# Kernel tuning notes

Hardware: AMD Instinct MI355X
Metric: run time of the kernel (lower is better)

The kernel has to match this reference:

```python
import jax, jax.numpy as jnp
import numpy as np

# pywt db4 reconstruction low-pass (rec_lo) coefficients.
_H = np.array([
    0.23037781330885523, 0.7148465705525415, 0.6308807679295904,
    -0.02798376941698385, -0.18703481171888114, 0.030841381835986965,
    0.032883011666982945, -0.010597401784997278], dtype=np.float64)
# pywt dec_lo = _H[::-1]; conv (flipped) correlation kernel = dec_lo[::-1] = _H.
_FLO = _H
# dec_hi[k] = (-1)^(7-k) * _H[k]; correlation kernel = dec_hi[::-1] -> (-1)^k * _H[7-k].
_FHI = np.array([(-1.0) ** k * _H[7 - k] for k in range(8)])
_FILT = jnp.asarray(np.stack([_FLO, _FHI])[:, None, :], dtype=jnp.float32)  # [2,1,8]
_PAD = 7  # filter_len - 1
_LEVEL = 4


def _dwt_step(sig):
    """One pywt dwt level, mode='symmetric'. sig: [N, L] -> (cA, cD), each [N, (L+7)//2]."""
    # symmetric (half-sample) extension by filter_len-1 each side, drop first sample
    # so that stride-2 VALID correlation reproduces pywt's output phase/length.
    xp = jnp.pad(sig, ((0, 0), (_PAD, _PAD)), mode='symmetric')[:, 1:]
    out = jax.lax.conv_general_dilated(
        xp[:, None, :], _FILT, window_strides=(2,), padding='VALID',
        dimension_numbers=('NCH', 'OIH', 'NCH'))  # [N, 2, (L+7)//2]
    return out[:, 0, :], out[:, 1, :]


def setup_inputs() -> dict:
    key = jax.random.key(0)
    x = jax.random.normal(key, (64, 4096, 32), dtype=jnp.float32)  # [B, L, C]
    return {"x": x}


def reference(x):
    """Faithful batched version of pywt.wavedec(x[i,:,j], 'db4', 'symmetric', level=4).
    Returns tuple (cA4, cD4, cD3, cD2, cD1), each [B, C, scale_len]."""
    B, L, C = x.shape
    sig = jnp.transpose(x, (0, 2, 1)).reshape(B * C, L)
    details = []
    for _ in range(_LEVEL):
        sig, cd = _dwt_step(sig)
        details.append(cd)
    coeffs = [sig] + details[::-1]  # [cA_L, cD_L, ..., cD_1] like pywt.wavedec
    return tuple(c.reshape(B, C, c.shape[-1]) for c in coeffs)
```

## Files before the change

### kernel.cpp

```cpp
#include <hip/hip_runtime.h>


#define NCH 8

__device__ __forceinline__ int sym_idx(int t, int L) {
    if (t < 0) t = -1 - t;
    if (t >= L) t = 2 * L - 1 - t;
    return t;
}

__device__ __forceinline__ void level_step(
    const float* __restrict__ src, int src_base, int srcL,
    float* __restrict__ dst, int dst_base,
    int lo, int hi,
    float* __restrict__ cdRow, int ownLo, int ownHi,
    float* __restrict__ caRow,
    int c, int slot) {
    constexpr float FLO[8] = {
        0.23037781330885523f,  0.7148465705525415f,  0.6308807679295904f,
        -0.02798376941698385f, -0.18703481171888114f, 0.030841381835986965f,
        0.032883011666982945f, -0.010597401784997278f};
    constexpr float FHI[8] = {
        -0.010597401784997278f, -0.032883011666982945f, 0.030841381835986965f,
        0.18703481171888114f,  -0.02798376941698385f,  -0.6308807679295904f,
        0.7148465705525415f,   -0.23037781330885523f};

    for (int i = lo + slot; i < hi; i += 32) {
        float a = 0.f, d = 0.f;
#pragma unroll
        for (int k = 0; k < 8; ++k) {
            int t = sym_idx(2 * i - 6 + k, srcL);
            const float v = src[(t - src_base) * NCH + c];
            a = fmaf(FLO[k], v, a);
            d = fmaf(FHI[k], v, d);
        }
        if (dst) dst[(i - dst_base) * NCH + c] = a;
        if (caRow) caRow[i] = a;
        if (i >= ownLo && i < ownHi) cdRow[i] = d;
    }
}

__global__ __launch_bounds__(256) void fused_dwt_kernel(
    const float* __restrict__ x, float* __restrict__ out) {
    const int bid = blockIdx.x;
    const int work = (bid & 7) * 256 + (bid >> 3);
    const int cg = work & 3;
    const int tile = (work >> 2) & 7;
    const int b = work >> 5;

    const int tid = threadIdx.x;
    const int c = tid & 7;
    const int slot = tid >> 3;
    const int c0 = cg * 8;

    const int L0 = 4096, L1 = 2051, L2 = 1029, L3 = 518, L4 = 262;

    const int lo4 = tile * 33, hi4 = min(L4, lo4 + 33);
    const int lo3 = max(0, 2 * lo4 - 6), hi3 = min(L3, 2 * hi4);
    const int lo2 = max(0, 2 * lo3 - 6), hi2 = min(L2, 2 * hi3);
    const int lo1 = max(0, 2 * lo2 - 6), hi1 = min(L1, 2 * hi2);
    const int lox = max(0, 2 * lo1 - 6), hix = min(L0, 2 * hi1);

    __shared__ float bx[618 * NCH];
    __shared__ float b1[306 * NCH];
    __shared__ float b2[150 * NCH];
    __shared__ float b3[72 * NCH];

    const float* xb = x + (size_t)b * L0 * 32 + c0;
    const int nx = hix - lox;
    for (int q = tid; q < nx * 2; q += 256) {
        const int jj = q >> 1;
        const int h = (q & 1) * 4;
        const float4 v = *reinterpret_cast<const float4*>(xb + (size_t)(lox + jj) * 32 + h);
        *reinterpret_cast<float4*>(&bx[jj * NCH + h]) = v;
    }
    __syncthreads();

    const size_t S = 2048;
    float* outCA4 = out;
    float* outCD4 = out + S * (size_t)L4;
    float* outCD3 = out + 2 * S * (size_t)L4;
    float* outCD2 = out + 2 * S * (size_t)L4 + S * (size_t)L3;
    float* outCD1 = out + 2 * S * (size_t)L4 + S * (size_t)L3 + S * (size_t)L2;

    const size_t sig = (size_t)b * 32 + c0 + c;

    const int o1lo = tile * 264, o1hi = min(L1, o1lo + 264);
    const int o2lo = tile * 132, o2hi = min(L2, o2lo + 132);
    const int o3lo = tile * 66, o3hi = min(L3, o3lo + 66);

    level_step(bx, lox, L0, b1, lo1, lo1, hi1,
               outCD1 + sig * L1, o1lo, o1hi, nullptr, c, slot);
    __syncthreads();
    level_step(b1, lo1, L1, b2, lo2, lo2, hi2,
               outCD2 + sig * L2, o2lo, o2hi, nullptr, c, slot);
    __syncthreads();
    level_step(b2, lo2, L2, b3, lo3, lo3, hi3,
               outCD3 + sig * L3, o3lo, o3hi, nullptr, c, slot);
    __syncthreads();
    level_step(b3, lo3, L3, nullptr, 0, lo4, hi4,
               outCD4 + sig * L4, lo4, hi4, outCA4 + sig * L4, c, slot);
}

extern "C" void kernel_launch(void* const* d_in, const int* in_sizes, int n_in,
                              void* d_out, int out_size, void* d_ws, size_t ws_size,
                              hipStream_t stream) {
    const float* x = (const float*)d_in[0];
    float* out = (float*)d_out;
    fused_dwt_kernel<<<dim3(2048), dim3(256), 0, stream>>>(x, out);
}
```

Before: 32.56 us.

## Use channel-major padded shared buffers with sliding-window register reuse per thread

Shared-memory staging moves from interleaved [sample][channel] to per-channel padded rows, and the symmetric boundary extension is written once into the padding. That removes the per-tap sym_idx branches. Each thread now computes R consecutive outputs and keeps a sliding window of float2 registers, so every input is read once instead of eight times. Output ownership ranges for the detail coefficients are also reassigned. This cuts LDS traffic and index arithmetic but adds bank-conflict risk from the strided row layout and more complex boundary logic.

Result: slower. 34.22 us (+5.1%).

```diff
diff --git a/kernel.cpp b/kernel.cpp
--- a/kernel.cpp
+++ b/kernel.cpp
@@ -2,20 +2,18 @@
 
 
 #define NCH 8
+#define LPX 634
+#define LP1 322
+#define LP2 166
+#define LP3 86
 
-__device__ __forceinline__ int sym_idx(int t, int L) {
-    if (t < 0) t = -1 - t;
-    if (t >= L) t = 2 * L - 1 - t;
-    return t;
-}
-
-__device__ __forceinline__ void level_step(
-    const float* __restrict__ src, int src_base, int srcL,
-    float* __restrict__ dst, int dst_base,
+template <int R, bool LAST>
+__device__ __forceinline__ void level_run(
+    const float* __restrict__ src, int LPS, int srclo,
+    float* __restrict__ dst, int LPD, int DL,
     int lo, int hi,
-    float* __restrict__ cdRow, int ownLo, int ownHi,
-    float* __restrict__ caRow,
-    int c, int slot) {
+    float* __restrict__ gcd, int ownLo, int ownHi,
+    float* __restrict__ gca, int c, int slot) {
     constexpr float FLO[8] = {
         0.23037781330885523f,  0.7148465705525415f,  0.6308807679295904f,
         -0.02798376941698385f, -0.18703481171888114f, 0.030841381835986965f,
@@ -25,23 +23,50 @@
         0.18703481171888114f,  -0.02798376941698385f,  -0.6308807679295904f,
         0.7148465705525415f,   -0.23037781330885523f};
 
-    for (int i = lo + slot; i < hi; i += 32) {
-        float a = 0.f, d = 0.f;
+    const int span = hi - lo;
+    int i0r = slot * R;
+    if (i0r > span - R) i0r = span - R;
+    const int i0 = lo + i0r;
+
+    const float2* row2 = reinterpret_cast<const float2*>(src + c * LPS);
+    int p = i0 - (srclo >> 1);
+    float2 f0 = row2[p], f1 = row2[p + 1], f2 = row2[p + 2];
+    float* drow = LAST ? nullptr : dst + c * LPD;
+
 #pragma unroll
-        for (int k = 0; k < 8; ++k) {
-            int t = sym_idx(2 * i - 6 + k, srcL);
-            const float v = src[(t - src_base) * NCH + c];
-            a = fmaf(FLO[k], v, a);
-            d = fmaf(FHI[k], v, d);
+    for (int r = 0; r < R; ++r) {
+        const float2 f3 = row2[p + 3 + r];
+        const int i = i0 + r;
+        const float w0 = f0.x, w1 = f0.y, w2 = f1.x, w3 = f1.y;
+        const float w4 = f2.x, w5 = f2.y, w6 = f3.x, w7 = f3.y;
+        float a = FLO[0] * w0;
+        a = fmaf(FLO[1], w1, a); a = fmaf(FLO[2], w2, a); a = fmaf(FLO[3], w3, a);
+        a = fmaf(FLO[4], w4, a); a = fmaf(FLO[5], w5, a); a = fmaf(FLO[6], w6, a);
+        a = fmaf(FLO[7], w7, a);
+        float d = FHI[0] * w0;
+        d = fmaf(FHI[1], w1, d); d = fmaf(FHI[2], w2, d); d = fmaf(FHI[3], w3, d);
+        d = fmaf(FHI[4], w4, d); d = fmaf(FHI[5], w5, d); d = fmaf(FHI[6], w6, d);
+        d = fmaf(FHI[7], w7, d);
+
+        if constexpr (!LAST) {
+            drow[i - lo + 6] = a;
+            if (lo == 0 && i < 6) drow[5 - i] = a;
+            if (hi == DL && i >= DL - 7) drow[(2 * DL - 1 - i) - lo + 6] = a;
+        } else {
+            gca[i] = a;
         }
-        if (dst) dst[(i - dst_base) * NCH + c] = a;
-        if (caRow) caRow[i] = a;
-        if (i >= ownLo && i < ownHi) cdRow[i] = d;
+        if (i >= ownLo && i < ownHi) gcd[i] = d;
+        f0 = f1; f1 = f2; f2 = f3;
     }
 }
 
 __global__ __launch_bounds__(256) void fused_dwt_kernel(
     const float* __restrict__ x, float* __restrict__ out) {
+    __shared__ __align__(16) float bx[NCH * LPX];
+    __shared__ __align__(16) float b1[NCH * LP1];
+    __shared__ __align__(16) float b2[NCH * LP2];
+    __shared__ __align__(16) float b3[NCH * LP3];
+
     const int bid = blockIdx.x;
     const int work = (bid & 7) * 256 + (bid >> 3);
     const int cg = work & 3;
@@ -61,45 +86,46 @@
     const int lo1 = max(0, 2 * lo2 - 6), hi1 = min(L1, 2 * hi2);
     const int lox = max(0, 2 * lo1 - 6), hix = min(L0, 2 * hi1);
 
-    __shared__ float bx[618 * NCH];
-    __shared__ float b1[306 * NCH];
-    __shared__ float b2[150 * NCH];
-    __shared__ float b3[72 * NCH];
-
     const float* xb = x + (size_t)b * L0 * 32 + c0;
     const int nx = hix - lox;
     for (int q = tid; q < nx * 2; q += 256) {
         const int jj = q >> 1;
         const int h = (q & 1) * 4;
-        const float4 v = *reinterpret_cast<const float4*>(xb + (size_t)(lox + jj) * 32 + h);
-        *reinterpret_cast<float4*>(&bx[jj * NCH + h]) = v;
+        const int t = lox + jj;
+        const float4 v = *reinterpret_cast<const float4*>(xb + (size_t)t * 32 + h);
+        const float vv[4] = {v.x, v.y, v.z, v.w};
+#pragma unroll
+        for (int hh = 0; hh < 4; ++hh) {
+            float* row = bx + (h + hh) * LPX;
+            row[jj + 6] = vv[hh];
+            if (lox == 0 && t < 6) row[5 - t] = vv[hh];
+            if (hix == L0 && t >= L0 - 7) row[(2 * L0 - 1 - t) - lox + 6] = vv[hh];
+        }
     }
     __syncthreads();
 
     const size_t S = 2048;
-    float* outCA4 = out;
-    float* outCD4 = out + S * (size_t)L4;
-    float* outCD3 = out + 2 * S * (size_t)L4;
-    float* outCD2 = out + 2 * S * (size_t)L4 + S * (size_t)L3;
-    float* outCD1 = out + 2 * S * (size_t)L4 + S * (size_t)L3 + S * (size_t)L2;
+    const size_t sig = (size_t)b * 32 + c0 + c;
+    float* gca4 = out + sig * L4;
+    float* gcd4 = out + S * (size_t)L4 + sig * L4;
+    float* gcd3 = out + 2 * S * (size_t)L4 + sig * L3;
+    float* gcd2 = out + 2 * S * (size_t)L4 + S * (size_t)L3 + sig * L2;
+    float* gcd1 = out + 2 * S * (size_t)L4 + S * (size_t)L3 + S * (size_t)L2 + sig * L1;
 
-    const size_t sig = (size_t)b * 32 + c0 + c;
+    const int o1lo = tile ? 264 * tile - 34 : 0;
+    const int o1hi = (tile == 7) ? L1 : 264 * tile + 230;
+    const int o2lo = tile ? 132 * tile - 10 : 0;
+    const int o2hi = (tile == 7) ? L2 : 132 * tile + 122;
+    const int o3lo = tile ? 66 * tile - 2 : 0;
+    const int o3hi = (tile == 7) ? L3 : 66 * tile + 64;
 
-    const int o1lo = tile * 264, o1hi = min(L1, o1lo + 264);
-    const int o2lo = tile * 132, o2hi = min(L2, o2lo + 132);
-    const int o3lo = tile * 66, o3hi = min(L3, o3lo + 66);
-
-    level_step(bx, lox, L0, b1, lo1, lo1, hi1,
-               outCD1 + sig * L1, o1lo, o1hi, nullptr, c, slot);
+    level_run<10, false>(bx, LPX, lox, b1, LP1, L1, lo1, hi1, gcd1, o1lo, o1hi, nullptr, c, slot);
     __syncthreads();
-    level_step(b1, lo1, L1, b2, lo2, lo2, hi2,
-               outCD2 + sig * L2, o2lo, o2hi, nullptr, c, slot);
+    level_run<5, false>(b1, LP1, lo1, b2, LP2, L2, lo2, hi2, gcd2, o2lo, o2hi, nullptr, c, slot);
     __syncthreads();
-    level_step(b2, lo2, L2, b3, lo3, lo3, hi3,
-               outCD3 + sig * L3, o3lo, o3hi, nullptr, c, slot);
+    level_run<3, false>(b2, LP2, lo2, b3, LP3, L3, lo3, hi3, gcd3, o3lo, o3hi, nullptr, c, slot);
     __syncthreads();
-    level_step(b3, lo3, L3, nullptr, 0, lo4, hi4,
-               outCD4 + sig * L4, lo4, hi4, outCA4 + sig * L4, c, slot);
+    level_run<2, true>(b3, LP3, lo3, nullptr, 0, L4, lo4, hi4, gcd4, lo4, hi4, gca4, c, slot);
 }
 
 extern "C" void kernel_launch(void* const* d_in, const int* in_sizes, int n_in,
```
